# Performance work log

Hardware: AMD Instinct MI355X
Metric: run time of the kernel (lower is better)

Reference implementation:

```python
import jax, jax.numpy as jnp
import numpy as np

MAX_LEVELS = 5
CHANNELS = 3


def _gauss_kernel(channels=CHANNELS):
    k = np.array([[1., 4., 6., 4., 1.],
                  [4., 16., 24., 16., 4.],
                  [6., 24., 36., 24., 6.],
                  [4., 16., 24., 16., 4.],
                  [1., 4., 6., 4., 1.]], dtype=np.float32) / 256.0
    return jnp.asarray(np.tile(k[None, None], (channels, 1, 1, 1)))  # (C,1,5,5)


def conv_gauss(img, kernel):
    # reflect-pad by 2 then depthwise 5x5 conv (groups = C)
    img = jnp.pad(img, ((0, 0), (0, 0), (2, 2), (2, 2)), mode='reflect')
    return jax.lax.conv_general_dilated(
        img, kernel, window_strides=(1, 1), padding='VALID',
        dimension_numbers=('NCHW', 'OIHW', 'NCHW'),
        feature_group_count=img.shape[1])


def downsample(x):
    return x[:, :, ::2, ::2]


def upsample(x, kernel):
    # zero-stuff: x at even (h,w) positions, zeros elsewhere, then smooth with 4*kernel
    b, c, h, w = x.shape
    up = jnp.zeros((b, c, 2 * h, 2 * w), dtype=x.dtype).at[:, :, ::2, ::2].set(x)
    return conv_gauss(up, 4.0 * kernel)


def laplacian_pyramid(img, kernel, max_levels=MAX_LEVELS):
    current = img
    pyr = []
    for _ in range(max_levels):
        filtered = conv_gauss(current, kernel)
        down = downsample(filtered)
        up = upsample(down, kernel)
        pyr.append(current - up)
        current = down
    return pyr


def setup_inputs() -> dict:
    key = jax.random.key(0)
    k1, k2 = jax.random.split(key)
    shape = (32, 3, 512, 512)
    return {
        'input': jax.random.normal(k1, shape, dtype=jnp.float32),
        'target': jax.random.normal(k2, shape, dtype=jnp.float32),
        'kernel': _gauss_kernel(CHANNELS),
    }


def reference(input, target, kernel):
    pyr_in = laplacian_pyramid(input, kernel, MAX_LEVELS)
    pyr_tg = laplacian_pyramid(target, kernel, MAX_LEVELS)
    # F.l1_loss default reduction: mean over all elements, per level
    return sum(jnp.mean(jnp.abs(a - b)) for a, b in zip(pyr_in, pyr_tg))
```

## Files before the change

kernel.cpp:

```cpp
#include <hip/hip_runtime.h>


#define BC 96
#define KA 0.0625f
#define KB 0.25f
#define KC 0.375f

__device__ __forceinline__ int refl(int i, int n) {
    if (i < 0) i = -i;
    if (i >= n) i = 2 * n - 2 - i;
    return i;
}

template<int SS, int NC, bool DIFF>
__device__ __forceinline__ void load_raw(const float* __restrict__ pa,
                                         const float* __restrict__ pb,
                                         int r, int basec,
                                         float* __restrict__ a,
                                         float* __restrict__ b) {
    const int off = r * SS + basec;
    if constexpr (NC == 8) {
        float4 a0 = *(const float4*)(pa + off);
        float4 a1 = *(const float4*)(pa + off + 4);
        a[0]=a0.x; a[1]=a0.y; a[2]=a0.z; a[3]=a0.w;
        a[4]=a1.x; a[5]=a1.y; a[6]=a1.z; a[7]=a1.w;
        if constexpr (DIFF) {
            float4 b0 = *(const float4*)(pb + off);
            float4 b1 = *(const float4*)(pb + off + 4);
            b[0]=b0.x; b[1]=b0.y; b[2]=b0.z; b[3]=b0.w;
            b[4]=b1.x; b[5]=b1.y; b[6]=b1.z; b[7]=b1.w;
        }
    } else if constexpr (NC == 4) {
        float4 a0 = *(const float4*)(pa + off);
        a[0]=a0.x; a[1]=a0.y; a[2]=a0.z; a[3]=a0.w;
        if constexpr (DIFF) {
            float4 b0 = *(const float4*)(pb + off);
            b[0]=b0.x; b[1]=b0.y; b[2]=b0.z; b[3]=b0.w;
        }
    } else {
        float2 a0 = *(const float2*)(pa + off);
        a[0]=a0.x; a[1]=a0.y;
        if constexpr (DIFF) {
            float2 b0 = *(const float2*)(pb + off);
            b[0]=b0.x; b[1]=b0.y;
        }
    }
}

template<int NC, bool DIFF>
__device__ __forceinline__ void materialize(const float* __restrict__ a,
                                            const float* __restrict__ b,
                                            float* __restrict__ c) {
#pragma unroll
    for (int i = 0; i < NC; ++i) c[i] = DIFF ? (a[i] - b[i]) : a[i];
}

template<int NC>
__device__ __forceinline__ void hconv(const float* __restrict__ c,
                                      float* __restrict__ o, int lane) {
    constexpr int ND = NC / 2;
    float e[NC + 3];
#pragma unroll
    for (int i = 0; i < NC; ++i) e[i + 2] = c[i];
    const bool l0 = (lane == 0), l63 = (lane == 63);
    { float v = __shfl(e[NC + 1], lane - 1); e[1] = l0 ? e[3] : v; }
    if constexpr (NC >= 4) {
        { float v = __shfl(e[NC], lane - 1); e[0] = l0 ? e[4] : v; }
        { float v = __shfl(e[2], lane + 1); e[NC + 2] = l63 ? e[NC] : v; }
    } else {
        e[0] = __shfl(e[2], l0 ? 1 : lane - 1);
        e[NC + 2] = __shfl(e[2], l63 ? 63 : lane + 1);
    }
#pragma unroll
    for (int j = 0; j < ND; ++j)
        o[j] = KA * e[2*j] + KB * e[2*j+1] + KC * e[2*j+2]
             + KB * e[2*j+3] + KA * e[2*j+4];
}

template<int H, int NC, int R, int SS, int DS, bool DIFF, int PD>
__device__ __forceinline__ float slide_strip(
        const float* __restrict__ pa, const float* __restrict__ pb,
        float* __restrict__ pd, int lane, int y0) {
    constexpr int ND = NC / 2;
    const int basec = lane * NC;

    float h0[ND], h1[ND], h2[ND], h3[ND], h4[ND];
    float wPrev[NC], pA[NC], pB[NC], pC[NC];
    float UA1[NC], UA2[NC];
    float UB1[DIFF ? NC : 1], UB2[DIFF ? NC : 1];
    float VA1[PD == 2 ? NC : 1], VA2[PD == 2 ? NC : 1];
    float VB1[(PD == 2 && DIFF) ? NC : 1], VB2[(PD == 2 && DIFF) ? NC : 1];
#pragma unroll
    for (int i = 0; i < NC; ++i) {
        wPrev[i] = 0.f; pA[i] = 0.f; pB[i] = 0.f; pC[i] = 0.f;
    }
    float acc = 0.f;

    const int d0 = y0 >> 1;
    const int db = d0 - 1;

    {
        float t[NC], tb[DIFF ? NC : 1], c[NC];
        load_raw<SS,NC,DIFF>(pa, pb, refl(2*db - 2, H), basec, t, tb);
        materialize<NC,DIFF>(t, tb, c); hconv<NC>(c, h0, lane);
        load_raw<SS,NC,DIFF>(pa, pb, refl(2*db - 1, H), basec, t, tb);
        materialize<NC,DIFF>(t, tb, c); hconv<NC>(c, h1, lane);
        load_raw<SS,NC,DIFF>(pa, pb, refl(2*db, H), basec, t, tb);
        materialize<NC,DIFF>(t, tb, c); hconv<NC>(c, h2, lane);
    }
    load_raw<SS,NC,DIFF>(pa, pb, refl(2*db + 1, H), basec, UA1, UB1);
    load_raw<SS,NC,DIFF>(pa, pb, refl(2*db + 2, H), basec, UA2, UB2);
    if constexpr (PD == 2) {
        load_raw<SS,NC,DIFF>(pa, pb, refl(2*db + 3, H), basec, VA1, VB1);
        load_raw<SS,NC,DIFF>(pa, pb, refl(2*db + 4, H), basec, VA2, VB2);
    }

    auto body = [&](int d, float* A1, float* A2, float* B1, float* B2,
                    bool doFin, bool doStore, bool doIssue) {
        float c1[NC], c2[NC];
        materialize<NC,DIFF>(A1, B1, c1);
        materialize<NC,DIFF>(A2, B2, c2);
        if (doIssue) {
            load_raw<SS,NC,DIFF>(pa, pb, refl(2*d + 2*PD + 1, H), basec, A1, B1);
            load_raw<SS,NC,DIFF>(pa, pb, refl(2*d + 2*PD + 2, H), basec, A2, B2);
        }
        hconv<NC>(c1, h3, lane);
        hconv<NC>(c2, h4, lane);

        float dn[ND];
#pragma unroll
        for (int j = 0; j < ND; ++j)
            dn[j] = KA*h0[j] + KB*h1[j] + KC*h2[j] + KB*h3[j] + KA*h4[j];

        if (doStore) {
            const int doff = d * DS + lane * ND;
            if constexpr (ND == 4) {
                float4 s; s.x=dn[0]; s.y=dn[1]; s.z=dn[2]; s.w=dn[3];
                *(float4*)(pd + doff) = s;
            } else if constexpr (ND == 2) {
                float2 s; s.x=dn[0]; s.y=dn[1];
                *(float2*)(pd + doff) = s;
            } else {
                pd[doff] = dn[0];
            }
        }

        float dm, dp;
        if constexpr (ND >= 2) {
            { float v = __shfl(dn[ND-1], lane - 1); dm = (lane == 0)  ? dn[1]    : v; }
            { float v = __shfl(dn[0],    lane + 1); dp = (lane == 63) ? dn[ND-1] : v; }
        } else {
            dm = __shfl(dn[0], (lane == 0)  ? 1  : lane - 1);
            dp = __shfl(dn[0], (lane == 63) ? 63 : lane + 1);
        }
        float wN[NC];
#pragma unroll
        for (int j = 0; j < ND; ++j) {
            float lf = j ? dn[j-1] : dm;
            float rg = (j + 1 < ND) ? dn[j+1] : dp;
            wN[2*j]     = 0.125f * lf + 0.75f * dn[j] + 0.125f * rg;
            wN[2*j + 1] = 0.5f * (dn[j] + rg);
        }

        if (doFin) {
#pragma unroll
            for (int i = 0; i < NC; ++i) {
                acc += fabsf(pA[i] - (0.75f*wPrev[i] + 0.125f*wN[i]));
                acc += fabsf(pB[i] - 0.5f*wN[i]);
            }
        }

#pragma unroll
        for (int i = 0; i < NC; ++i) {
            pA[i] = pC[i];
            pC[i] = c2[i] - 0.125f * wN[i];
            pB[i] = c1[i] - 0.5f   * wN[i];
            wPrev[i] = wN[i];
        }
#pragma unroll
        for (int j = 0; j < ND; ++j) { h0[j] = h2[j]; h1[j] = h3[j]; h2[j] = h4[j]; }
    };

    if constexpr (PD == 1) {
#pragma unroll
        for (int k = 0; k < R/2 + 2; ++k) {
            body(db + k, UA1, UA2, UB1, UB2,
                 k >= 2,
                 k >= 1 && k < R/2 + 1,
                 k < R/2 + 1);
        }
    } else {
        constexpr int CNT2 = R / 4 + 1;
#pragma unroll
        for (int i = 0; i < CNT2; ++i) {
            const bool fin = (i >= 1);
            const bool iss = (i < CNT2 - 1);
            body(db + 2*i,     UA1, UA2, UB1, UB2, fin, i >= 1,       iss);
            body(db + 2*i + 1, VA1, VA2, VB1, VB2, fin, i < CNT2 - 1, iss);
        }
    }
    return acc;
}

template<int H, int NC, bool DIFF, int R>
__global__ __launch_bounds__(256) void lap_slide(
        const float* __restrict__ A, const float* __restrict__ B,
        float* __restrict__ down, float* __restrict__ out, float invN) {
    constexpr int Hd = H / 2, SPP = H / R;
    __shared__ float red[4];
    const int tid = threadIdx.x;
    const int lane = tid & 63, wid = tid >> 6;
    const int sid = blockIdx.x * 4 + wid;
    const int bc = sid / SPP;
    const int y0 = (sid % SPP) * R;
    const float* pa = A + (size_t)bc * H * H;
    const float* pb = DIFF ? (B + (size_t)bc * H * H) : nullptr;
    float* pd = down + (size_t)bc * Hd * Hd;

    float acc = slide_strip<H, NC, R, H, Hd, DIFF, 2>(pa, pb, pd, lane, y0);

#pragma unroll
    for (int off2 = 32; off2 > 0; off2 >>= 1)
        acc += __shfl_down(acc, off2, 64);
    if (lane == 0) red[wid] = acc;
    __syncthreads();
    if (tid == 0)
        atomicAdd(out, (red[0] + red[1] + red[2] + red[3]) * invN);
}

__global__ __launch_bounds__(1024) void lap_rest(
        const float* __restrict__ down0, float* __restrict__ out,
        float invN1, float invN2, float invN3, float invN4) {
    __shared__ float d1[128 * 128];
    __shared__ float p[64 * 66];
    __shared__ float hh[64 * 34];
    __shared__ float dd[32 * 34];
    __shared__ float W3[32 * 64];
    __shared__ float h4[32 * 18];
    __shared__ float d4[16 * 18];
    __shared__ float W4[16 * 32];
    __shared__ float red[16];
    const int tid = threadIdx.x;
    const int lane = tid & 63, wid = tid >> 6;
    const float* src = down0 + (size_t)blockIdx.x * 65536;

    float acc = invN1 *
        slide_strip<256, 4, 16, 256, 128, false, 1>(src, nullptr, d1, lane, wid * 16);
    __syncthreads();
    acc += invN2 *
        slide_strip<128, 2, 8, 128, 66, false, 1>(d1, nullptr, p, lane, wid * 8);
    __syncthreads();

    const float k[5] = {KA, KB, KC, KB, KA};
    for (int i = tid; i < 64 * 32; i += 1024) {
        int r = i >> 5, t = i & 31;
        const float* pr = p + r * 66;
        float s = 0.f;
#pragma unroll
        for (int v = 0; v < 5; ++v) s += k[v] * pr[refl(2*t + v - 2, 64)];
        hh[r * 34 + t] = s;
    }
    __syncthreads();
    for (int i = tid; i < 32 * 32; i += 1024) {
        int dy = i >> 5, t = i & 31;
        float s = 0.f;
#pragma unroll
        for (int u = 0; u < 5; ++u) s += k[u] * hh[refl(2*dy + u - 2, 64) * 34 + t];
        dd[dy * 34 + t] = s;
    }
    __syncthreads();
    for (int i = tid; i < 32 * 32; i += 1024) {
        int a = i >> 5, t = i & 31;
        const float* dr = dd + a * 34;
        float dm = dr[t == 0 ? 1 : t - 1];
        float dc = dr[t];
        float dp = dr[t == 31 ? 31 : t + 1];
        W3[a * 64 + 2*t]     = 0.125f * dm + 0.75f * dc + 0.125f * dp;
        W3[a * 64 + 2*t + 1] = 0.5f * (dc + dp);
    }
    __syncthreads();
    float acc3 = 0.f;
    for (int i = tid; i < 4096; i += 1024) {
        int y = i >> 6, x = i & 63;
        float cur = p[y * 66 + x];
        float up;
        if ((y & 1) == 0) {
            int a0 = refl(y - 2, 64) >> 1, a1 = y >> 1, a2 = refl(y + 2, 64) >> 1;
            up = 0.125f*W3[a0*64 + x] + 0.75f*W3[a1*64 + x] + 0.125f*W3[a2*64 + x];
        } else {
            int a0 = (y - 1) >> 1, a1 = refl(y + 1, 64) >> 1;
            up = 0.5f * (W3[a0*64 + x] + W3[a1*64 + x]);
        }
        acc3 += fabsf(cur - up);
    }
    __syncthreads();
    for (int i = tid; i < 32 * 16; i += 1024) {
        int r = i >> 4, t = i & 15;
        const float* pr = dd + r * 34;
        float s = 0.f;
#pragma unroll
        for (int v = 0; v < 5; ++v) s += k[v] * pr[refl(2*t + v - 2, 32)];
        h4[r * 18 + t] = s;
    }
    __syncthreads();
    for (int i = tid; i < 16 * 16; i += 1024) {
        int dy = i >> 4, t = i & 15;
        float s = 0.f;
#pragma unroll
        for (int u = 0; u < 5; ++u) s += k[u] * h4[refl(2*dy + u - 2, 32) * 18 + t];
        d4[dy * 18 + t] = s;
    }
    __syncthreads();
    for (int i = tid; i < 16 * 16; i += 1024) {
        int a = i >> 4, t = i & 15;
        const float* dr = d4 + a * 18;
        float dm = dr[t == 0 ? 1 : t - 1];
        float dc = dr[t];
        float dp = dr[t == 15 ? 15 : t + 1];
        W4[a * 32 + 2*t]     = 0.125f * dm + 0.75f * dc + 0.125f * dp;
        W4[a * 32 + 2*t + 1] = 0.5f * (dc + dp);
    }
    __syncthreads();
    float acc4 = 0.f;
    for (int i = tid; i < 1024; i += 1024) {
        int y = i >> 5, x = i & 31;
        float cur = dd[y * 34 + x];
        float up;
        if ((y & 1) == 0) {
            int a0 = refl(y - 2, 32) >> 1, a1 = y >> 1, a2 = refl(y + 2, 32) >> 1;
            up = 0.125f*W4[a0*32 + x] + 0.75f*W4[a1*32 + x] + 0.125f*W4[a2*32 + x];
        } else {
            int a0 = (y - 1) >> 1, a1 = refl(y + 1, 32) >> 1;
            up = 0.5f * (W4[a0*32 + x] + W4[a1*32 + x]);
        }
        acc4 += fabsf(cur - up);
    }
    acc += acc3 * invN3 + acc4 * invN4;

#pragma unroll
    for (int off2 = 32; off2 > 0; off2 >>= 1)
        acc += __shfl_down(acc, off2, 64);
    if (lane == 0) red[wid] = acc;
    __syncthreads();
    if (tid == 0) {
        float s = 0.f;
#pragma unroll
        for (int i = 0; i < 16; ++i) s += red[i];
        atomicAdd(out, s);
    }
}

extern "C" void kernel_launch(void* const* d_in, const int* in_sizes, int n_in,
                              void* d_out, int out_size, void* d_ws, size_t ws_size,
                              hipStream_t stream) {
    const float* in = (const float*)d_in[0];
    const float* tg = (const float*)d_in[1];
    float* out = (float*)d_out;
    float* ws = (float*)d_ws;

    float* down0 = ws;

    hipMemsetAsync(out, 0, sizeof(float), stream);

    lap_slide<512, 8, true, 16><<<96 * 32 / 4, 256, 0, stream>>>(
        in, tg, down0, out, 1.f / (96.f * 512.f * 512.f));
    lap_rest<<<BC, 1024, 0, stream>>>(
        down0, out,
        1.f / (96.f * 256.f * 256.f), 1.f / (96.f * 128.f * 128.f),
        1.f / (96.f * 64.f * 64.f),  1.f / (96.f * 32.f * 32.f));
}
```

Before: 243.7 us.

## Stream level-0 rows through a double-buffered LDS ring via direct global-to-LDS loads

```diff
diff --git a/kernel.cpp b/kernel.cpp
--- a/kernel.cpp
+++ b/kernel.cpp
@@ -77,6 +77,143 @@
              + KB * e[2*j+3] + KA * e[2*j+4];
 }
 
+__device__ __forceinline__ void dma_half(const float* g, float* l, int lane) {
+    __builtin_amdgcn_global_load_lds(
+        (__attribute__((address_space(1))) const void*)(g + 4 * lane),
+        (__attribute__((address_space(3))) void*)(l), 16, 0, 0);
+}
+__device__ __forceinline__ void dma_row512(const float* g, float* l, int lane) {
+    dma_half(g, l, lane);
+    dma_half(g + 256, l + 256, lane);
+}
+__device__ __forceinline__ void dma_slot(const float* pa, const float* pb,
+                                         int r1, int r2, float* slot, int lane) {
+    dma_row512(pa + (size_t)r1 * 512, slot + 0 * 512, lane);
+    dma_row512(pa + (size_t)r2 * 512, slot + 1 * 512, lane);
+    dma_row512(pb + (size_t)r1 * 512, slot + 2 * 512, lane);
+    dma_row512(pb + (size_t)r2 * 512, slot + 3 * 512, lane);
+}
+__device__ __forceinline__ void lds_row8(const float* l, int lane, float* c) {
+    const float4 x = *(const float4*)(l + lane * 8);
+    const float4 y = *(const float4*)(l + lane * 8 + 4);
+    c[0]=x.x; c[1]=x.y; c[2]=x.z; c[3]=x.w;
+    c[4]=y.x; c[5]=y.y; c[6]=y.z; c[7]=y.w;
+}
+
+__global__ __launch_bounds__(256) void lap0_dma(
+        const float* __restrict__ A, const float* __restrict__ B,
+        float* __restrict__ down, float* __restrict__ out, float invN) {
+    constexpr int H = 512, Hd = 256, R = 32, SPP = H / R;
+    constexpr int NB = R / 2 + 2;
+    __shared__ float ring[4][2][4][512];
+    __shared__ float red[4];
+    const int tid = threadIdx.x;
+    const int lane = tid & 63, wid = tid >> 6;
+    const int sid = blockIdx.x * 4 + wid;
+    const int bc = sid / SPP;
+    const int y0 = (sid % SPP) * R;
+    const float* pa = A + (size_t)bc * H * H;
+    const float* pb = B + (size_t)bc * H * H;
+    float* pd = down + (size_t)bc * Hd * Hd;
+    float* slot0 = &ring[wid][0][0][0];
+    float* slot1 = &ring[wid][1][0][0];
+    const int basec = lane * 8;
+
+    const int d0 = y0 >> 1;
+    const int db = d0 - 1;
+
+    float h0[4], h1[4], h2[4], h3[4], h4[4];
+    float wPrev[8], pA[8], pB[8], pC[8];
+#pragma unroll
+    for (int i = 0; i < 8; ++i) { wPrev[i]=0.f; pA[i]=0.f; pB[i]=0.f; pC[i]=0.f; }
+    float acc = 0.f;
+
+    {
+        float t[8], tb[8], c[8];
+        load_raw<H,8,true>(pa, pb, refl(2*db - 2, H), basec, t, tb);
+        materialize<8,true>(t, tb, c); hconv<8>(c, h0, lane);
+        load_raw<H,8,true>(pa, pb, refl(2*db - 1, H), basec, t, tb);
+        materialize<8,true>(t, tb, c); hconv<8>(c, h1, lane);
+        load_raw<H,8,true>(pa, pb, refl(2*db, H), basec, t, tb);
+        materialize<8,true>(t, tb, c); hconv<8>(c, h2, lane);
+    }
+    dma_slot(pa, pb, refl(2*db + 1, H), refl(2*db + 2, H), slot0, lane);
+    dma_slot(pa, pb, refl(2*db + 3, H), refl(2*db + 4, H), slot1, lane);
+
+#pragma unroll
+    for (int k = 0; k < NB; ++k) {
+        const int d = db + k;
+        float* slot = (k & 1) ? slot1 : slot0;
+
+        asm volatile("s_waitcnt vmcnt(8)" ::: "memory");
+
+        float a1[8], a2[8], b1[8], b2[8], c1[8], c2[8];
+        lds_row8(slot + 0 * 512, lane, a1);
+        lds_row8(slot + 1 * 512, lane, a2);
+        lds_row8(slot + 2 * 512, lane, b1);
+        lds_row8(slot + 3 * 512, lane, b2);
+#pragma unroll
+        for (int i = 0; i < 8; ++i) { c1[i] = a1[i] - b1[i]; c2[i] = a2[i] - b2[i]; }
+
+        hconv<8>(c1, h3, lane);
+        hconv<8>(c2, h4, lane);
+
+        float dn[4];
+#pragma unroll
+        for (int j = 0; j < 4; ++j)
+            dn[j] = KA*h0[j] + KB*h1[j] + KC*h2[j] + KB*h3[j] + KA*h4[j];
+
+        if (k >= 1 && k < 1 + R/2) {
+            const int doff = d * Hd + lane * 4;
+            float4 s; s.x=dn[0]; s.y=dn[1]; s.z=dn[2]; s.w=dn[3];
+            *(float4*)(pd + doff) = s;
+        }
+
+        float dm, dp;
+        { float v = __shfl(dn[3], lane - 1); dm = (lane == 0)  ? dn[1] : v; }
+        { float v = __shfl(dn[0], lane + 1); dp = (lane == 63) ? dn[3] : v; }
+        float wN[8];
+#pragma unroll
+        for (int j = 0; j < 4; ++j) {
+            float lf = j ? dn[j-1] : dm;
+            float rg = (j + 1 < 4) ? dn[j+1] : dp;
+            wN[2*j]     = 0.125f * lf + 0.75f * dn[j] + 0.125f * rg;
+            wN[2*j + 1] = 0.5f * (dn[j] + rg);
+        }
+
+        if (k >= 2) {
+#pragma unroll
+            for (int i = 0; i < 8; ++i) {
+                acc += fabsf(pA[i] - (0.75f*wPrev[i] + 0.125f*wN[i]));
+                acc += fabsf(pB[i] - 0.5f*wN[i]);
+            }
+        }
+
+#pragma unroll
+        for (int i = 0; i < 8; ++i) {
+            pA[i] = pC[i];
+            pC[i] = c2[i] - 0.125f * wN[i];
+            pB[i] = c1[i] - 0.5f   * wN[i];
+            wPrev[i] = wN[i];
+        }
+#pragma unroll
+        for (int j = 0; j < 4; ++j) { h0[j] = h2[j]; h1[j] = h3[j]; h2[j] = h4[j]; }
+
+        if (k < NB - 2) {
+            asm volatile("s_waitcnt lgkmcnt(0)" ::: "memory");
+            dma_slot(pa, pb, refl(2*d + 5, H), refl(2*d + 6, H), slot, lane);
+        }
+    }
+
+#pragma unroll
+    for (int off2 = 32; off2 > 0; off2 >>= 1)
+        acc += __shfl_down(acc, off2, 64);
+    if (lane == 0) red[wid] = acc;
+    __syncthreads();
+    if (tid == 0)
+        atomicAdd(out, (red[0] + red[1] + red[2] + red[3]) * invN);
+}
+
 template<int H, int NC, int R, int SS, int DS, bool DIFF, int PD>
 __device__ __forceinline__ float slide_strip(
         const float* __restrict__ pa, const float* __restrict__ pb,
@@ -200,32 +337,6 @@
         }
     }
     return acc;
-}
-
-template<int H, int NC, bool DIFF, int R>
-__global__ __launch_bounds__(256) void lap_slide(
-        const float* __restrict__ A, const float* __restrict__ B,
-        float* __restrict__ down, float* __restrict__ out, float invN) {
-    constexpr int Hd = H / 2, SPP = H / R;
-    __shared__ float red[4];
-    const int tid = threadIdx.x;
-    const int lane = tid & 63, wid = tid >> 6;
-    const int sid = blockIdx.x * 4 + wid;
-    const int bc = sid / SPP;
-    const int y0 = (sid % SPP) * R;
-    const float* pa = A + (size_t)bc * H * H;
-    const float* pb = DIFF ? (B + (size_t)bc * H * H) : nullptr;
-    float* pd = down + (size_t)bc * Hd * Hd;
-
-    float acc = slide_strip<H, NC, R, H, Hd, DIFF, 2>(pa, pb, pd, lane, y0);
-
-#pragma unroll
-    for (int off2 = 32; off2 > 0; off2 >>= 1)
-        acc += __shfl_down(acc, off2, 64);
-    if (lane == 0) red[wid] = acc;
-    __syncthreads();
-    if (tid == 0)
-        atomicAdd(out, (red[0] + red[1] + red[2] + red[3]) * invN);
 }
 
 __global__ __launch_bounds__(1024) void lap_rest(
@@ -362,7 +473,7 @@
 
     hipMemsetAsync(out, 0, sizeof(float), stream);
 
-    lap_slide<512, 8, true, 16><<<96 * 32 / 4, 256, 0, stream>>>(
+    lap0_dma<<<96 * 16 / 4, 256, 0, stream>>>(
         in, tg, down0, out, 1.f / (96.f * 512.f * 512.f));
     lap_rest<<<BC, 1024, 0, stream>>>(
         down0, out,
```

Result: slower. 250.3 us (+2.7%).

## Split level-0 strips into two column halves with halo edge loads and block swizzle

Applied to the files above, without the earlier changes.

```diff
diff --git a/kernel.cpp b/kernel.cpp
--- a/kernel.cpp
+++ b/kernel.cpp
@@ -77,6 +77,157 @@
              + KB * e[2*j+3] + KA * e[2*j+4];
 }
 
+__global__ __launch_bounds__(256) void lap0_cs(
+        const float* __restrict__ A, const float* __restrict__ B,
+        float* __restrict__ down, float* __restrict__ out, float invN) {
+    constexpr int H = 512, Hd = 256, R = 16;
+    constexpr int NB = R / 2 + 2;
+    __shared__ float red[4];
+    const int tid = threadIdx.x;
+    const int lane = tid & 63, wid = tid >> 6;
+    const int bid = blockIdx.x;
+    const int wg = (bid & 7) * 192 + (bid >> 3);
+    const int sid = wg * 4 + wid;
+    const int bc = sid >> 6;
+    const int rem = sid & 63;
+    const int strip = rem >> 1;
+    const int sw = rem & 1;
+    const int y0 = strip * R;
+    const int x0 = sw << 8;
+    const int ecol = 256 - 4 * sw;
+    const float* pa = A + (size_t)bc * H * H;
+    const float* pb = B + (size_t)bc * H * H;
+    float* pd = down + (size_t)bc * Hd * Hd;
+    const int basec = x0 + lane * 4;
+
+    float h0[2], h1[2], h2[2], h3[2], h4[2];
+    float hE0, hE1, hE2, hE3, hE4;
+    float wPrev[4], pA_[4], pB_[4], pC_[4];
+    float UA1[4], UA2[4], UB1[4], UB2[4];
+    float4 EA1, EA2, EB1, EB2;
+#pragma unroll
+    for (int i = 0; i < 4; ++i) { wPrev[i]=0.f; pA_[i]=0.f; pB_[i]=0.f; pC_[i]=0.f; }
+    float acc = 0.f;
+
+    const int d0 = y0 >> 1;
+    const int db = d0 - 1;
+
+    auto hconv_cs = [&](const float* c, const float4& eD, float* o, float& hE) {
+        float e[7];
+        e[2]=c[0]; e[3]=c[1]; e[4]=c[2]; e[5]=c[3];
+        const bool l0 = (lane == 0), l63 = (lane == 63);
+        { float v = __shfl(e[5], lane - 1); e[1] = l0 ? (sw ? eD.w : e[3]) : v; }
+        { float v = __shfl(e[4], lane - 1); e[0] = l0 ? (sw ? eD.z : e[4]) : v; }
+        { float v = __shfl(e[2], lane + 1); e[6] = l63 ? (sw ? e[4] : eD.x) : v; }
+        o[0] = KA*e[0] + KB*e[1] + KC*e[2] + KB*e[3] + KA*e[4];
+        o[1] = KA*e[2] + KB*e[3] + KC*e[4] + KB*e[5] + KA*e[6];
+        float hA = KA*c[2] + KB*c[3] + KC*eD.x + KB*eD.y + KA*eD.z;
+        float hB = KA*eD.x + KB*eD.y + KC*eD.z + KB*eD.w + KA*c[0];
+        hE = sw ? hB : hA;
+    };
+
+    auto load_edge = [&](int r) -> float4 {
+        const float4 ea = *(const float4*)(pa + r * H + ecol);
+        const float4 eb = *(const float4*)(pb + r * H + ecol);
+        float4 d; d.x=ea.x-eb.x; d.y=ea.y-eb.y; d.z=ea.z-eb.z; d.w=ea.w-eb.w;
+        return d;
+    };
+
+    {
+        float t[4], tb[4], c[4];
+        int r = refl(2*db - 2, H);
+        load_raw<H,4,true>(pa, pb, r, basec, t, tb);
+        materialize<4,true>(t, tb, c);
+        hconv_cs(c, load_edge(r), h0, hE0);
+        r = refl(2*db - 1, H);
+        load_raw<H,4,true>(pa, pb, r, basec, t, tb);
+        materialize<4,true>(t, tb, c);
+        hconv_cs(c, load_edge(r), h1, hE1);
+        r = refl(2*db, H);
+        load_raw<H,4,true>(pa, pb, r, basec, t, tb);
+        materialize<4,true>(t, tb, c);
+        hconv_cs(c, load_edge(r), h2, hE2);
+    }
+    {
+        const int r1 = refl(2*db + 1, H), r2 = refl(2*db + 2, H);
+        load_raw<H,4,true>(pa, pb, r1, basec, UA1, UB1);
+        load_raw<H,4,true>(pa, pb, r2, basec, UA2, UB2);
+        EA1 = *(const float4*)(pa + r1 * H + ecol);
+        EB1 = *(const float4*)(pb + r1 * H + ecol);
+        EA2 = *(const float4*)(pa + r2 * H + ecol);
+        EB2 = *(const float4*)(pb + r2 * H + ecol);
+    }
+
+#pragma unroll
+    for (int k = 0; k < NB; ++k) {
+        const int d = db + k;
+        float c1[4], c2[4];
+#pragma unroll
+        for (int i = 0; i < 4; ++i) { c1[i] = UA1[i] - UB1[i]; c2[i] = UA2[i] - UB2[i]; }
+        float4 eD1, eD2;
+        eD1.x=EA1.x-EB1.x; eD1.y=EA1.y-EB1.y; eD1.z=EA1.z-EB1.z; eD1.w=EA1.w-EB1.w;
+        eD2.x=EA2.x-EB2.x; eD2.y=EA2.y-EB2.y; eD2.z=EA2.z-EB2.z; eD2.w=EA2.w-EB2.w;
+        if (k < NB - 1) {
+            const int r1 = refl(2*d + 3, H), r2 = refl(2*d + 4, H);
+            load_raw<H,4,true>(pa, pb, r1, basec, UA1, UB1);
+            load_raw<H,4,true>(pa, pb, r2, basec, UA2, UB2);
+            EA1 = *(const float4*)(pa + r1 * H + ecol);
+            EB1 = *(const float4*)(pb + r1 * H + ecol);
+            EA2 = *(const float4*)(pa + r2 * H + ecol);
+            EB2 = *(const float4*)(pb + r2 * H + ecol);
+        }
+
+        hconv_cs(c1, eD1, h3, hE3);
+        hconv_cs(c2, eD2, h4, hE4);
+
+        float dn[2];
+        dn[0] = KA*h0[0] + KB*h1[0] + KC*h2[0] + KB*h3[0] + KA*h4[0];
+        dn[1] = KA*h0[1] + KB*h1[1] + KC*h2[1] + KB*h3[1] + KA*h4[1];
+        const float dnE = KA*hE0 + KB*hE1 + KC*hE2 + KB*hE3 + KA*hE4;
+
+        if (k >= 1 && k < 1 + R/2) {
+            const int doff = d * Hd + (sw << 7) + lane * 2;
+            float2 s; s.x = dn[0]; s.y = dn[1];
+            *(float2*)(pd + doff) = s;
+        }
+
+        float dm, dp;
+        { float v = __shfl(dn[1], lane - 1); dm = (lane == 0)  ? (sw ? dnE : dn[1]) : v; }
+        { float v = __shfl(dn[0], lane + 1); dp = (lane == 63) ? (sw ? dn[1] : dnE) : v; }
+        float wN[4];
+        wN[0] = 0.125f*dm    + 0.75f*dn[0] + 0.125f*dn[1];
+        wN[1] = 0.5f*(dn[0] + dn[1]);
+        wN[2] = 0.125f*dn[0] + 0.75f*dn[1] + 0.125f*dp;
+        wN[3] = 0.5f*(dn[1] + dp);
+
+        if (k >= 2) {
+#pragma unroll
+            for (int i = 0; i < 4; ++i) {
+                acc += fabsf(pA_[i] - (0.75f*wPrev[i] + 0.125f*wN[i]));
+                acc += fabsf(pB_[i] - 0.5f*wN[i]);
+            }
+        }
+
+#pragma unroll
+        for (int i = 0; i < 4; ++i) {
+            pA_[i] = pC_[i];
+            pC_[i] = c2[i] - 0.125f * wN[i];
+            pB_[i] = c1[i] - 0.5f   * wN[i];
+            wPrev[i] = wN[i];
+        }
+        h0[0]=h2[0]; h0[1]=h2[1]; h1[0]=h3[0]; h1[1]=h3[1]; h2[0]=h4[0]; h2[1]=h4[1];
+        hE0 = hE2; hE1 = hE3; hE2 = hE4;
+    }
+
+#pragma unroll
+    for (int off2 = 32; off2 > 0; off2 >>= 1)
+        acc += __shfl_down(acc, off2, 64);
+    if (lane == 0) red[wid] = acc;
+    __syncthreads();
+    if (tid == 0)
+        atomicAdd(out, (red[0] + red[1] + red[2] + red[3]) * invN);
+}
+
 template<int H, int NC, int R, int SS, int DS, bool DIFF, int PD>
 __device__ __forceinline__ float slide_strip(
         const float* __restrict__ pa, const float* __restrict__ pb,
@@ -200,32 +351,6 @@
         }
     }
     return acc;
-}
-
-template<int H, int NC, bool DIFF, int R>
-__global__ __launch_bounds__(256) void lap_slide(
-        const float* __restrict__ A, const float* __restrict__ B,
-        float* __restrict__ down, float* __restrict__ out, float invN) {
-    constexpr int Hd = H / 2, SPP = H / R;
-    __shared__ float red[4];
-    const int tid = threadIdx.x;
-    const int lane = tid & 63, wid = tid >> 6;
-    const int sid = blockIdx.x * 4 + wid;
-    const int bc = sid / SPP;
-    const int y0 = (sid % SPP) * R;
-    const float* pa = A + (size_t)bc * H * H;
-    const float* pb = DIFF ? (B + (size_t)bc * H * H) : nullptr;
-    float* pd = down + (size_t)bc * Hd * Hd;
-
-    float acc = slide_strip<H, NC, R, H, Hd, DIFF, 2>(pa, pb, pd, lane, y0);
-
-#pragma unroll
-    for (int off2 = 32; off2 > 0; off2 >>= 1)
-        acc += __shfl_down(acc, off2, 64);
-    if (lane == 0) red[wid] = acc;
-    __syncthreads();
-    if (tid == 0)
-        atomicAdd(out, (red[0] + red[1] + red[2] + red[3]) * invN);
 }
 
 __global__ __launch_bounds__(1024) void lap_rest(
@@ -362,7 +487,7 @@
 
     hipMemsetAsync(out, 0, sizeof(float), stream);
 
-    lap_slide<512, 8, true, 16><<<96 * 32 / 4, 256, 0, stream>>>(
+    lap0_cs<<<6144 / 4, 256, 0, stream>>>(
         in, tg, down0, out, 1.f / (96.f * 512.f * 512.f));
     lap_rest<<<BC, 1024, 0, stream>>>(
         down0, out,
```

Result: slower. 251.7 us (+3.3%).
